# Performance work log

Measured on AMD Instinct MI355X. Metric: run time of the kernel, lower is better.

The kernel has to match this reference:

```python
import jax, jax.numpy as jnp
import numpy as np

N = 100_000      # nodes
E = 1_200_000    # edges per graph (avg degree 12)
D = 64           # args.hidden
PROP_STEP = 8
LAM = 1.0
ALP = 1.0 / (LAM + 1.0)   # args.alp <= 0 -> 1/(lam+1)
LAM0 = 1.0
K = 4
LAM_K = 0.5


def setup_inputs() -> dict:
    key = jax.random.key(0)
    k0, k1, k2, k3, k4 = jax.random.split(key, 5)
    x = jax.random.normal(k0, (N, D), dtype=jnp.float32)
    src0 = jax.random.randint(k1, (E,), 0, N, dtype=jnp.int32)
    # ensure every node has in-degree >= 1 (no isolated dst nodes)
    dst0 = jnp.concatenate([jnp.arange(N, dtype=jnp.int32),
                            jax.random.randint(k2, (E - N,), 0, N, dtype=jnp.int32)])
    src1 = jax.random.randint(k3, (E,), 0, N, dtype=jnp.int32)
    dst1 = jnp.concatenate([jnp.arange(N, dtype=jnp.int32),
                            jax.random.randint(k4, (E - N,), 0, N, dtype=jnp.int32)])
    return {"x": x, "src0": src0, "dst0": dst0, "src1": src1, "dst1": dst1}


def _in_degrees(dst):
    # DGL in_degrees(): count of incoming edges per node
    return jax.ops.segment_sum(jnp.ones(dst.shape, jnp.float32), dst, num_segments=N)


def _normalized_AX(src, dst, inv_sqrt_deg, Y):
    # Y <- D^{-1/2} A D^{-1/2} Y  (edge weight w = 1)
    Yn = Y * inv_sqrt_deg                                    # [N, D]
    agg = jax.ops.segment_sum(Yn[src], dst, num_segments=N)  # gather/scatter SpMM
    return agg * inv_sqrt_deg


def reference(x, src0, dst0, src1, dst1):
    deg0 = _in_degrees(dst0)
    deg1 = _in_degrees(dst1)
    # D^{-1/2} with inf -> 0 (as in D_power_X)
    inv0 = jnp.where(deg0 > 0, deg0 ** -0.5, 0.0)[:, None]
    inv1 = jnp.where(deg1 > 0, deg1 ** -0.5, 0.0)[:, None]
    D0 = deg0[:, None]
    D1 = deg1[:, None]
    Y = x
    for _ in range(PROP_STEP):
        nAX0 = _normalized_AX(src0, dst0, inv0, Y)
        nAX1 = _normalized_AX(src1, dst1, inv1, Y)
        Y = Y - ALP * (LAM0 * (Y - x) / (D0 + D1)
                       + LAM * (Y - nAX0)
                       - (LAM_K / K) * (Y - nAX1))
    return Y
```

## Files before the change

kernel.cpp:

```cpp
#include <hip/hip_runtime.h>
#include <hip/hip_fp16.h>

#define NN 100000
#define NE 1200000
#define DIM 64
#define NBINS 391
#define NBE 128
#define CHUNK (NE / NBE)
#define NBLK ((NN + 255) / 256)
#define NPH 7


__global__ void __launch_bounds__(256) bin_count(const int* __restrict__ dst0,
                                                 const int* __restrict__ dst1,
                                                 int* __restrict__ blk_cnt) {
    __shared__ int c[NBINS];
    int t = threadIdx.x;
    for (int i = t; i < NBINS; i += 256) c[i] = 0;
    __syncthreads();
    int lo = blockIdx.x * CHUNK, hi = lo + CHUNK;
    for (int e = lo + t; e < hi; e += 256) {
        atomicAdd(&c[dst0[e] >> 8], 1);
        atomicAdd(&c[dst1[e] >> 8], 1);
    }
    __syncthreads();
    for (int i = t; i < NBINS; i += 256) blk_cnt[blockIdx.x * NBINS + i] = c[i];
}

__global__ void __launch_bounds__(512) bin_scan(const int* __restrict__ blk_cnt,
                                                int* __restrict__ bin_start) {
    __shared__ int tot[512];
    int t = threadIdx.x;
    int s = 0;
    if (t < NBINS)
        for (int b = 0; b < NBE; ++b) s += blk_cnt[b * NBINS + t];
    tot[t] = s;
    __syncthreads();
    for (int off = 1; off < 512; off <<= 1) {
        int v = (t >= off) ? tot[t - off] : 0;
        __syncthreads();
        tot[t] += v;
        __syncthreads();
    }
    if (t <= NBINS) bin_start[t] = tot[t] - s;
}

__global__ void __launch_bounds__(NBE) blk_base_k(const int* __restrict__ blk_cnt,
                                                  const int* __restrict__ bin_start,
                                                  int* __restrict__ blk_base) {
    __shared__ int s[NBE];
    int b = blockIdx.x, t = threadIdx.x;
    int v = blk_cnt[t * NBINS + b];
    s[t] = v;
    __syncthreads();
    for (int off = 1; off < NBE; off <<= 1) {
        int x = (t >= off) ? s[t - off] : 0;
        __syncthreads();
        s[t] += x;
        __syncthreads();
    }
    blk_base[t * NBINS + b] = bin_start[b] + s[t] - v;
}

__global__ void __launch_bounds__(256) bin_permute(const int* __restrict__ src0,
                                                   const int* __restrict__ dst0,
                                                   const int* __restrict__ src1,
                                                   const int* __restrict__ dst1,
                                                   const int* __restrict__ blk_base,
                                                   unsigned int* __restrict__ binned) {
    __shared__ int off[NBINS];
    int t = threadIdx.x;
    for (int i = t; i < NBINS; i += 256) off[i] = blk_base[blockIdx.x * NBINS + i];
    __syncthreads();
    int lo = blockIdx.x * CHUNK, hi = lo + CHUNK;
    for (int e = lo + t; e < hi; e += 256) {
        int s = src0[e], d = dst0[e];
        int p = atomicAdd(&off[d >> 8], 1);
        binned[p] = (unsigned)s | ((unsigned)(d & 255) << 18);
        s = src1[e]; d = dst1[e];
        p = atomicAdd(&off[d >> 8], 1);
        binned[p] = (unsigned)s | (1u << 17) | ((unsigned)(d & 255) << 18);
    }
}

__global__ void __launch_bounds__(256) deg_count(const unsigned int* __restrict__ binned,
                                                 const int* __restrict__ bin_start,
                                                 int* __restrict__ deg0,
                                                 int* __restrict__ deg1) {
    __shared__ int dg[512];
    int b = blockIdx.x, t = threadIdx.x;
    dg[t] = 0; dg[t + 256] = 0;
    __syncthreads();
    int lo = bin_start[b], hi = bin_start[b + 1];
    for (int i = lo + t; i < hi; i += 256) {
        unsigned r = binned[i];
        int dlow = (r >> 18) & 255, g = (r >> 17) & 1;
        atomicAdd(&dg[(dlow << 1) | g], 1);
    }
    __syncthreads();
    int n = b * 256 + t;
    if (n < NN) { deg0[n] = dg[t << 1]; deg1[n] = dg[(t << 1) | 1]; }
}

__global__ void __launch_bounds__(256) scan_l1(const int* __restrict__ deg0,
                                               const int* __restrict__ deg1,
                                               int* __restrict__ rs, int* __restrict__ dp,
                                               int* __restrict__ bs) {
    __shared__ int s0[256];
    int t = threadIdx.x;
    int n = blockIdx.x * 256 + t;
    int a = 0;
    if (n < NN) a = (deg0[n] + deg1[n] + 7) & ~7;
    s0[t] = a;
    __syncthreads();
    for (int off = 1; off < 256; off <<= 1) {
        int x0 = (t >= off) ? s0[t - off] : 0;
        __syncthreads();
        s0[t] += x0;
        __syncthreads();
    }
    if (n < NN) { rs[n] = s0[t] - a; dp[n] = a; }
    if (t == 255) bs[blockIdx.x] = s0[255];
}

__global__ void __launch_bounds__(512) scan_l2(int* __restrict__ bs) {
    __shared__ int s0[512];
    int t = threadIdx.x;
    int a = (t < NBLK) ? bs[t] : 0;
    s0[t] = a;
    __syncthreads();
    for (int off = 1; off < 512; off <<= 1) {
        int x0 = (t >= off) ? s0[t - off] : 0;
        __syncthreads();
        s0[t] += x0;
        __syncthreads();
    }
    if (t < NBLK) bs[t] = s0[t] - a;
}

__global__ void __launch_bounds__(256) scan_l3(int* __restrict__ rs, const int* __restrict__ bs) {
    int n = blockIdx.x * 256 + threadIdx.x;
    if (n < NN) rs[n] += bs[blockIdx.x];
}

__global__ void node_params(const int* __restrict__ deg0, const int* __restrict__ deg1,
                            float2* __restrict__ nsc, float* __restrict__ sc,
                            float* __restrict__ cy) {
    int n = blockIdx.x * blockDim.x + threadIdx.x;
    if (n < NN) {
        int a = deg0[n], b = deg1[n];
        nsc[n] = make_float2((a > 0) ? 0.5f * rsqrtf((float)a) : 0.0f,
                             (b > 0) ? -0.0625f * rsqrtf((float)b) : 0.0f);
        int s = a + b;
        float rD = (s > 0) ? 1.0f / (float)s : 0.0f;
        sc[n] = 0.5625f - 0.5f * rD;
        cy[n] = 0.5f * rD;
    }
}

__global__ void __launch_bounds__(256) csr_scatter(const unsigned int* __restrict__ binned,
                                                   const int* __restrict__ bin_start,
                                                   const int* __restrict__ rs,
                                                   const int* __restrict__ deg0,
                                                   const int* __restrict__ deg1,
                                                   int* __restrict__ es) {
    __shared__ int hist[8 * 256];
    __shared__ int rsl[256];
    __shared__ int degsum[256];
    int b = blockIdx.x, t = threadIdx.x;
    int n = b * 256 + t;
    rsl[t] = (n < NN) ? rs[n] : 0;
    for (int i = t; i < 8 * 256; i += 256) hist[i] = 0;
    __syncthreads();
    int lo = bin_start[b], hi = bin_start[b + 1];
    for (int i = lo + t; i < hi; i += 256) {
        unsigned r = binned[i];
        int ph = (r & 0x1FFFF) >> 14;
        atomicAdd(&hist[ph * 256 + ((r >> 18) & 255)], 1);
    }
    __syncthreads();
    {
        int acc = 0;
        for (int ph = 0; ph < NPH; ++ph) {
            int v = hist[ph * 256 + t];
            hist[ph * 256 + t] = acc;
            acc += v;
        }
        degsum[t] = acc;
    }
    __syncthreads();
    for (int i = lo + t; i < hi; i += 256) {
        unsigned r = binned[i];
        int sN = r & 0x1FFFF, g = (r >> 17) & 1, dlow = (r >> 18) & 255;
        int ph = sN >> 14;
        int p = atomicAdd(&hist[ph * 256 + dlow], 1);
        int dgv = g ? deg1[sN] : deg0[sN];
        es[rsl[dlow] + p] = sN | (g << 17) | (dgv << 18);
    }
    __syncthreads();
    if (n < NN) {
        int base = rsl[t], ds = degsum[t], dpv = (ds + 7) & ~7;
        for (int i = base + ds; i < base + dpv; ++i) es[i] = 0;
    }
}

__global__ void convert_x(const float* __restrict__ X, const float* __restrict__ cy,
                          __half* __restrict__ HA, __half* __restrict__ BX) {
    int i = blockIdx.x * blockDim.x + threadIdx.x;
    if (i < NN * DIM / 4) {
        float4 v = ((const float4*)X)[i];
        float c = cy[i >> 4];
        ushort4 a, b;
        a.x = __half_as_ushort(__float2half(v.x));
        a.y = __half_as_ushort(__float2half(v.y));
        a.z = __half_as_ushort(__float2half(v.z));
        a.w = __half_as_ushort(__float2half(v.w));
        b.x = __half_as_ushort(__float2half(v.x * c));
        b.y = __half_as_ushort(__float2half(v.y * c));
        b.z = __half_as_ushort(__float2half(v.z * c));
        b.w = __half_as_ushort(__float2half(v.w * c));
        ((ushort4*)HA)[i] = a;
        ((ushort4*)BX)[i] = b;
    }
}

__global__ void __launch_bounds__(256) step_kernel(
    const __half* __restrict__ Yh, const __half* __restrict__ BX,
    const int* __restrict__ rs, const int* __restrict__ dp,
    const int* __restrict__ es, const float2* __restrict__ nsc,
    const float* __restrict__ sc,
    __half* __restrict__ Yho, float* __restrict__ Ffo)
{
    __shared__ float lut[128];
    for (int i = threadIdx.x; i < 128; i += 256)
        lut[i] = (i == 0) ? 0.0f : rsqrtf((float)i);
    __syncthreads();

    int node = blockIdx.x * 4 + (threadIdx.x >> 6);
    int d = threadIdx.x & 63;
    int un = __builtin_amdgcn_readfirstlane(node);
    int s  = __builtin_amdgcn_readfirstlane(rs[un]);
    int c  = __builtin_amdgcn_readfirstlane(dp[un]);
    float2 ns = nsc[un];

    float acc = 0.0f;
    int eb[8];
#pragma unroll
    for (int k = 0; k < 8; ++k) eb[k] = es[s + k];
    for (int i = 0; i < c; i += 8) {
        int en[8];
#pragma unroll
        for (int k = 0; k < 8; ++k) en[k] = es[s + i + 8 + k];
        float yv[8];
#pragma unroll
        for (int k = 0; k < 8; ++k)
            yv[k] = __half2float(Yh[(size_t)(eb[k] & 0x1FFFF) * DIM + d]);
#pragma unroll
        for (int k = 0; k < 8; ++k) {
            float wsc = (eb[k] & (1 << 17)) ? ns.y : ns.x;
            acc = fmaf(yv[k], wsc * lut[eb[k] >> 18], acc);
        }
#pragma unroll
        for (int k = 0; k < 8; ++k) eb[k] = en[k];
    }
    float y  = __half2float(Yh[(size_t)un * DIM + d]);
    float bx = __half2float(BX[(size_t)un * DIM + d]);
    float o = fmaf(sc[un], y, bx) + acc;
    if (Ffo) Ffo[(size_t)un * DIM + d] = o;
    else     Yho[(size_t)un * DIM + d] = __float2half(o);
}

extern "C" void kernel_launch(void* const* d_in, const int* in_sizes, int n_in,
                              void* d_out, int out_size, void* d_ws, size_t ws_size,
                              hipStream_t stream) {
    const float* x   = (const float*)d_in[0];
    const int* src0  = (const int*)d_in[1];
    const int* dst0  = (const int*)d_in[2];
    const int* src1  = (const int*)d_in[3];
    const int* dst1  = (const int*)d_in[4];
    float* out = (float*)d_out;

    char* ws = (char*)d_ws;
    size_t off = 0;
    auto alloc = [&](size_t bytes) -> void* {
        void* p = ws + off;
        off += (bytes + 255) & ~(size_t)255;
        return p;
    };

    const size_t ES_CAP = (size_t)2 * NE + 8 * NN + 64;

    __half* HA   = (__half*)alloc((size_t)NN * DIM * 2);
    __half* HB   = (__half*)alloc((size_t)NN * DIM * 2);
    __half* BX   = (__half*)alloc((size_t)NN * DIM * 2);
    unsigned int* binned = (unsigned int*)alloc((size_t)2 * NE * 4);
    int*    es   = (int*)alloc(ES_CAP * 4);
    int*    blk_cnt  = (int*)alloc((size_t)NBE * NBINS * 4);
    int*    blk_base = (int*)alloc((size_t)NBE * NBINS * 4);
    int*    bin_st   = (int*)alloc((size_t)(NBINS + 1) * 4);
    int*    deg0 = (int*)alloc((size_t)NN * 4);
    int*    deg1 = (int*)alloc((size_t)NN * 4);
    int*    rs   = (int*)alloc((size_t)NN * 4);
    int*    dp   = (int*)alloc((size_t)NN * 4);
    float2* nsc  = (float2*)alloc((size_t)NN * 8);
    float*  sc   = (float*)alloc((size_t)NN * 4);
    float*  cy   = (float*)alloc((size_t)NN * 4);
    int*    bs   = (int*)alloc((size_t)NBLK * 4);

    const int TB = 256;
    bin_count<<<NBE, 256, 0, stream>>>(dst0, dst1, blk_cnt);
    bin_scan<<<1, 512, 0, stream>>>(blk_cnt, bin_st);
    blk_base_k<<<NBINS, NBE, 0, stream>>>(blk_cnt, bin_st, blk_base);
    bin_permute<<<NBE, 256, 0, stream>>>(src0, dst0, src1, dst1, blk_base, binned);
    deg_count<<<NBINS, 256, 0, stream>>>(binned, bin_st, deg0, deg1);
    scan_l1<<<NBLK, 256, 0, stream>>>(deg0, deg1, rs, dp, bs);
    scan_l2<<<1, 512, 0, stream>>>(bs);
    scan_l3<<<NBLK, 256, 0, stream>>>(rs, bs);
    node_params<<<(NN + TB - 1) / TB, TB, 0, stream>>>(deg0, deg1, nsc, sc, cy);
    csr_scatter<<<NBINS, 256, 0, stream>>>(binned, bin_st, rs, deg0, deg1, es);
    convert_x<<<(NN * DIM / 4 + TB - 1) / TB, TB, 0, stream>>>(x, cy, HA, BX);

    int grid = NN / 4;
    for (int i = 0; i < 8; ++i) {
        const __half* hin = (i & 1) ? HB : HA;
        __half* hout = (i & 1) ? HA : HB;
        float* fout = (i == 7) ? out : nullptr;
        step_kernel<<<grid, TB, 0, stream>>>(hin, BX, rs, dp, es, nsc, sc, hout, fout);
    }
}
```

Measured before the change: 534.7 us.

## Split each wavefront into four edge groups with vectorized half4 row gathers

The step kernel now assigns four 16-lane subgroups of each wavefront to different edges, with each lane loading four fp16 features as a single 8-byte ushort4. Each subgroup handles two edges per iteration, and the partial sums are combined with cross-lane xor shuffles. This replaces the scalar 2-byte per-lane gathers, cutting the number of memory instructions per edge and raising load width. In exchange it adds a shuffle reduction and leaves three quarters of the lanes idle during the epilogue.

```diff
diff --git a/kernel.cpp b/kernel.cpp
--- a/kernel.cpp
+++ b/kernel.cpp
@@ -224,6 +224,13 @@
     }
 }
 
+__device__ __forceinline__ float4 h4f(ushort4 v) {
+    return make_float4(__half2float(__ushort_as_half(v.x)),
+                       __half2float(__ushort_as_half(v.y)),
+                       __half2float(__ushort_as_half(v.z)),
+                       __half2float(__ushort_as_half(v.w)));
+}
+
 __global__ void __launch_bounds__(256) step_kernel(
     const __half* __restrict__ Yh, const __half* __restrict__ BX,
     const int* __restrict__ rs, const int* __restrict__ dp,
@@ -237,37 +244,59 @@
     __syncthreads();
 
     int node = blockIdx.x * 4 + (threadIdx.x >> 6);
-    int d = threadIdx.x & 63;
+    int lane = threadIdx.x & 63;
+    int sub  = lane >> 4;
+    int fl   = lane & 15;
     int un = __builtin_amdgcn_readfirstlane(node);
     int s  = __builtin_amdgcn_readfirstlane(rs[un]);
     int c  = __builtin_amdgcn_readfirstlane(dp[un]);
     float2 ns = nsc[un];
 
-    float acc = 0.0f;
-    int eb[8];
-#pragma unroll
-    for (int k = 0; k < 8; ++k) eb[k] = es[s + k];
+    float4 acc = make_float4(0.0f, 0.0f, 0.0f, 0.0f);
+    int r0 = es[s + sub];
+    int r1 = es[s + 4 + sub];
     for (int i = 0; i < c; i += 8) {
-        int en[8];
-#pragma unroll
-        for (int k = 0; k < 8; ++k) en[k] = es[s + i + 8 + k];
-        float yv[8];
-#pragma unroll
-        for (int k = 0; k < 8; ++k)
-            yv[k] = __half2float(Yh[(size_t)(eb[k] & 0x1FFFF) * DIM + d]);
-#pragma unroll
-        for (int k = 0; k < 8; ++k) {
-            float wsc = (eb[k] & (1 << 17)) ? ns.y : ns.x;
-            acc = fmaf(yv[k], wsc * lut[eb[k] >> 18], acc);
+        int n0 = es[s + i + 8 + sub];
+        int n1 = es[s + i + 12 + sub];
+        ushort4 a0 = *(const ushort4*)(Yh + (size_t)(r0 & 0x1FFFF) * DIM + 4 * fl);
+        ushort4 a1 = *(const ushort4*)(Yh + (size_t)(r1 & 0x1FFFF) * DIM + 4 * fl);
+        float w0 = ((r0 & (1 << 17)) ? ns.y : ns.x) * lut[(unsigned)r0 >> 18];
+        float w1 = ((r1 & (1 << 17)) ? ns.y : ns.x) * lut[(unsigned)r1 >> 18];
+        float4 f0 = h4f(a0), f1 = h4f(a1);
+        acc.x = fmaf(f0.x, w0, acc.x);
+        acc.y = fmaf(f0.y, w0, acc.y);
+        acc.z = fmaf(f0.z, w0, acc.z);
+        acc.w = fmaf(f0.w, w0, acc.w);
+        acc.x = fmaf(f1.x, w1, acc.x);
+        acc.y = fmaf(f1.y, w1, acc.y);
+        acc.z = fmaf(f1.z, w1, acc.z);
+        acc.w = fmaf(f1.w, w1, acc.w);
+        r0 = n0; r1 = n1;
+    }
+    acc.x += __shfl_xor(acc.x, 16); acc.x += __shfl_xor(acc.x, 32);
+    acc.y += __shfl_xor(acc.y, 16); acc.y += __shfl_xor(acc.y, 32);
+    acc.z += __shfl_xor(acc.z, 16); acc.z += __shfl_xor(acc.z, 32);
+    acc.w += __shfl_xor(acc.w, 16); acc.w += __shfl_xor(acc.w, 32);
+
+    if (sub == 0) {
+        float4 y  = h4f(*(const ushort4*)(Yh + (size_t)un * DIM + 4 * fl));
+        float4 bx = h4f(*(const ushort4*)(BX + (size_t)un * DIM + 4 * fl));
+        float scl = sc[un];
+        float o0 = fmaf(scl, y.x, bx.x) + acc.x;
+        float o1 = fmaf(scl, y.y, bx.y) + acc.y;
+        float o2 = fmaf(scl, y.z, bx.z) + acc.z;
+        float o3 = fmaf(scl, y.w, bx.w) + acc.w;
+        if (Ffo) {
+            *(float4*)(Ffo + (size_t)un * DIM + 4 * fl) = make_float4(o0, o1, o2, o3);
+        } else {
+            ushort4 ov;
+            ov.x = __half_as_ushort(__float2half(o0));
+            ov.y = __half_as_ushort(__float2half(o1));
+            ov.z = __half_as_ushort(__float2half(o2));
+            ov.w = __half_as_ushort(__float2half(o3));
+            *(ushort4*)(Yho + (size_t)un * DIM + 4 * fl) = ov;
         }
-#pragma unroll
-        for (int k = 0; k < 8; ++k) eb[k] = en[k];
-    }
-    float y  = __half2float(Yh[(size_t)un * DIM + d]);
-    float bx = __half2float(BX[(size_t)un * DIM + d]);
-    float o = fmaf(sc[un], y, bx) + acc;
-    if (Ffo) Ffo[(size_t)un * DIM + d] = o;
-    else     Yho[(size_t)un * DIM + d] = __float2half(o);
+    }
 }
 
 extern "C" void kernel_launch(void* const* d_in, const int* in_sizes, int n_in,
```

Result: faster. 501.8 us (-6.2%).
